# Optimization experiments

Hardware: AMD Instinct MI355X
Metric: run time of the kernel (lower is better)

Reference implementation:

```python
import jax, jax.numpy as jnp
import numpy as np

TEMPERATURE = 0.7
TOP_K = 50
TOP_P = 0.9
B, S, H, V = 2, 1024, 512, 50257


def setup_inputs() -> dict:
    key = jax.random.key(0)
    k1, k2 = jax.random.split(key)
    x = jax.random.normal(k1, (B, S, H), dtype=jnp.float32)
    # small init scale keeps logits in a realistic range so nucleus mass is spread
    W = jax.random.normal(k2, (V, H), dtype=jnp.float32) * 0.02
    b = jnp.zeros((V,), dtype=jnp.float32)
    return {"x": x, "W": W, "b": b}


def _top_k_top_p_filtering(logits):
    # --- top-k: mask everything below the k-th largest value ---
    top_k_vals = jax.lax.top_k(logits, TOP_K)[0]          # [B,S,K]
    min_top_k = top_k_vals[..., -1:]                       # [B,S,1]
    logits = jnp.where(logits < min_top_k, -jnp.inf, logits)
    # --- top-p (nucleus): sort descending, cumsum of probs, drop tail ---
    sorted_idx = jnp.argsort(-logits, axis=-1)             # descending order
    sorted_logits = jnp.take_along_axis(logits, sorted_idx, axis=-1)
    cum_probs = jnp.cumsum(jax.nn.softmax(sorted_logits, axis=-1), axis=-1)
    sorted_logits = jnp.where(cum_probs > TOP_P, -jnp.inf, sorted_logits)
    # NOTE: the original torch code does gather(sorted_logits, index=sorted_indices)
    # (forward-gather, not inverse scatter). We replicate that exact math.
    logits = jnp.take_along_axis(sorted_logits, sorted_idx, axis=-1)
    return logits


def reference(x, W, b):
    # ExampleModel: single linear projection to vocab logits [B,S,V]
    logits = jnp.einsum('bsh,vh->bsv', x, W) + b
    logits = logits / TEMPERATURE
    filtered = _top_k_top_p_filtering(logits)
    return jax.nn.softmax(filtered, axis=-1)
```

## Files before the change

kernel.cpp:

```cpp
#include <hip/hip_runtime.h>
#include <math.h>

#define TEMP 0.7f
#define TOPK 50
#define TOPP 0.9f
#define M_TOT 2048
#define K_DIM 512
#define V_DIM 50257
#define NPAD 50304
#define KP 1536
#define BM 128
#define BN 128
#define BKE 64
#define NSTEP (KP / BKE)
#define NBN (NPAD / BN)
#define NBM (M_TOT / BM)

typedef short s16x8 __attribute__((ext_vector_type(8)));
typedef float f32x4 __attribute__((ext_vector_type(4)));

#define MFMA_16x16x32_BF16(acc, va, vb) \
  asm("v_mfma_f32_16x16x32_bf16 %0, %1, %2, %0" : "+v"(acc) : "v"(va), "v"(vb))

__device__ __forceinline__ unsigned short bf16_rn(float x) {
  unsigned u = __float_as_uint(x);
  unsigned r = u + 0x7FFFu + ((u >> 16) & 1u);
  return (unsigned short)(r >> 16);
}
__device__ __forceinline__ float bf16_to_f(unsigned short h) {
  return __uint_as_float(((unsigned)h) << 16);
}
__device__ __forceinline__ unsigned f2key(float f) {
  unsigned u = __float_as_uint(f);
  return (u & 0x80000000u) ? ~u : (u | 0x80000000u);
}

__global__ __launch_bounds__(256) void convx_kernel(const float* __restrict__ X,
                                                    unsigned short* __restrict__ Xp) {
  int idx = blockIdx.x * 256 + threadIdx.x;
  const int total = M_TOT * (K_DIM / 4);
  if (idx >= total) return;
  int row = idx >> 7;
  int q = idx & 127;
  const float4 v = reinterpret_cast<const float4*>(X)[idx];
  float vv[4] = {v.x, v.y, v.z, v.w};
  unsigned short hi[4], lo[4];
#pragma unroll
  for (int j = 0; j < 4; ++j) {
    hi[j] = bf16_rn(vv[j]);
    lo[j] = bf16_rn(vv[j] - bf16_to_f(hi[j]));
  }
  ushort4 h4 = make_ushort4(hi[0], hi[1], hi[2], hi[3]);
  ushort4 l4 = make_ushort4(lo[0], lo[1], lo[2], lo[3]);
  size_t base = (size_t)row * KP + q * 4;
  *reinterpret_cast<ushort4*>(Xp + base) = h4;
  *reinterpret_cast<ushort4*>(Xp + base + K_DIM) = h4;
  *reinterpret_cast<ushort4*>(Xp + base + 2 * K_DIM) = l4;
}

__global__ __launch_bounds__(256) void convw_kernel(const float* __restrict__ W,
                                                    unsigned short* __restrict__ Wp) {
  int idx = blockIdx.x * 256 + threadIdx.x;
  const int total = NPAD * (K_DIM / 4);
  if (idx >= total) return;
  int row = idx >> 7;
  int q = idx & 127;
  float4 v = make_float4(0.f, 0.f, 0.f, 0.f);
  if (row < V_DIM) v = reinterpret_cast<const float4*>(W)[(size_t)row * 128 + q];
  float vv[4] = {v.x, v.y, v.z, v.w};
  unsigned short hi[4], lo[4];
#pragma unroll
  for (int j = 0; j < 4; ++j) {
    hi[j] = bf16_rn(vv[j]);
    lo[j] = bf16_rn(vv[j] - bf16_to_f(hi[j]));
  }
  ushort4 h4 = make_ushort4(hi[0], hi[1], hi[2], hi[3]);
  ushort4 l4 = make_ushort4(lo[0], lo[1], lo[2], lo[3]);
  size_t base = (size_t)row * KP + q * 4;
  *reinterpret_cast<ushort4*>(Wp + base) = h4;
  *reinterpret_cast<ushort4*>(Wp + base + K_DIM) = l4;
  *reinterpret_cast<ushort4*>(Wp + base + 2 * K_DIM) = h4;
}

__global__ __launch_bounds__(256) void mfma_gemm_kernel(
    const unsigned short* __restrict__ Ap, const unsigned short* __restrict__ Bp,
    const float* __restrict__ Bv, float* __restrict__ C,
    unsigned* __restrict__ Tmax) {
  __shared__ __align__(16) unsigned char lds[32768];
  __shared__ unsigned umax[BM];
  const int tid = threadIdx.x;
  const int w = tid >> 6, lane = tid & 63;
  const int bm = blockIdx.x * BM;
  const int bni = blockIdx.y;
  const int bn = bni * BN;
  const int wr = w >> 1, wc = w & 1;

  f32x4 acc[4][4] = {};

  for (int step = 0; step < NSTEP; ++step) {
    const int k0 = step * BKE;
#pragma unroll
    for (int q = 0; q < 4; ++q) {
      int pp = ((w * 4 + q) << 10) + (lane << 4);
      int row = pp >> 7;
      int cb = (pp & 127) ^ ((row & 7) << 4);
      const unsigned short* ga = Ap + (size_t)(bm + row) * KP + k0 + (cb >> 1);
      __builtin_amdgcn_global_load_lds(
          (const __attribute__((address_space(1))) unsigned int*)ga,
          (__attribute__((address_space(3))) unsigned int*)(lds + pp), 16, 0, 0);
      const unsigned short* gb = Bp + (size_t)(bn + row) * KP + k0 + (cb >> 1);
      __builtin_amdgcn_global_load_lds(
          (const __attribute__((address_space(1))) unsigned int*)gb,
          (__attribute__((address_space(3))) unsigned int*)(lds + 16384 + pp), 16, 0, 0);
    }
    __syncthreads();
#pragma unroll
    for (int kk = 0; kk < 2; ++kk) {
      const int kbyte = kk * 64 + ((lane >> 4) << 4);
      s16x8 a[4], b[4];
#pragma unroll
      for (int i = 0; i < 4; ++i) {
        int row = (wr << 6) + (i << 4) + (lane & 15);
        int byte = (row << 7) + (kbyte ^ ((row & 7) << 4));
        a[i] = *reinterpret_cast<const s16x8*>(lds + byte);
      }
#pragma unroll
      for (int j = 0; j < 4; ++j) {
        int row = (wc << 6) + (j << 4) + (lane & 15);
        int byte = (row << 7) + (kbyte ^ ((row & 7) << 4));
        b[j] = *reinterpret_cast<const s16x8*>(lds + 16384 + byte);
      }
#pragma unroll
      for (int i = 0; i < 4; ++i)
#pragma unroll
        for (int j = 0; j < 4; ++j) MFMA_16x16x32_BF16(acc[i][j], a[i], b[j]);
    }
    __syncthreads();
  }

  if (tid < BM) umax[tid] = 0;
  __syncthreads();

  float mx[4][4];
#pragma unroll
  for (int i = 0; i < 4; ++i)
#pragma unroll
    for (int r = 0; r < 4; ++r) mx[i][r] = -INFINITY;

#pragma unroll
  for (int i = 0; i < 4; ++i) {
#pragma unroll
    for (int j = 0; j < 4; ++j) {
      int n = bn + (wc << 6) + (j << 4) + (lane & 15);
      if (n < V_DIM) {
        float bv = Bv[n];
#pragma unroll
        for (int r = 0; r < 4; ++r) {
          int m = bm + (wr << 6) + (i << 4) + ((lane >> 4) << 2) + r;
          float val = (acc[i][j][r] + bv) / TEMP;
          C[(size_t)m * V_DIM + n] = val;
          mx[i][r] = fmaxf(mx[i][r], val);
        }
      }
    }
  }
#pragma unroll
  for (int i = 0; i < 4; ++i) {
#pragma unroll
    for (int r = 0; r < 4; ++r) {
      float v = mx[i][r];
      v = fmaxf(v, __shfl_xor(v, 1));
      v = fmaxf(v, __shfl_xor(v, 2));
      v = fmaxf(v, __shfl_xor(v, 4));
      v = fmaxf(v, __shfl_xor(v, 8));
      if ((lane & 15) == 0)
        atomicMax(&umax[(wr << 6) + (i << 4) + ((lane >> 4) << 2) + r], f2key(v));
    }
  }
  __syncthreads();
  if (tid < BM) Tmax[(size_t)(bm + tid) * NBN + bni] = umax[tid];
}

#define CAP 1024
#define SCAP 256

__global__ __launch_bounds__(256) void select_kernel(float* __restrict__ C,
                                                     const unsigned* __restrict__ Tmax) {
  const int row = blockIdx.x;
  float* rowp = C + (size_t)row * V_DIM;
  const int tid = threadIdx.x;

  __shared__ unsigned tk[NBN];
  __shared__ short ctile[NBN];
  __shared__ unsigned s_t50;
  __shared__ float cval[CAP];
  __shared__ int cidx[CAP];
  __shared__ float sval[SCAP];
  __shared__ int sidx[SCAP];
  __shared__ float pvals[SCAP];
  __shared__ int s_cnt, s_ntile, s_nsurv, s_kc;
  __shared__ float s_invZ;

  for (int i = tid; i < NBN; i += 256) tk[i] = Tmax[(size_t)row * NBN + i];
  if (tid == 0) { s_cnt = 0; s_ntile = 0; s_nsurv = 0; }
  __syncthreads();
  for (int i = tid; i < NBN; i += 256) {
    unsigned ki = tk[i];
    int r = 0;
    for (int j = 0; j < NBN; ++j) {
      unsigned kj = tk[j];
      r += (kj > ki) || (kj == ki && j < i);
    }
    if (r == TOPK - 1) s_t50 = ki;
  }
  __syncthreads();
  const unsigned t50 = s_t50;

  for (int i = tid; i < NBN; i += 256) {
    if (tk[i] >= t50) {
      int p = atomicAdd(&s_ntile, 1);
      ctile[p] = (short)i;
    }
  }
  __syncthreads();
  const int ntile = s_ntile;

  for (int e = tid; e < ntile * BN; e += 256) {
    int ti = ctile[e >> 7];
    int n = ti * BN + (e & 127);
    if (n < V_DIM) {
      float l = rowp[n];
      if (f2key(l) >= t50) {
        int p = atomicAdd(&s_cnt, 1);
        if (p < CAP) { cval[p] = l; cidx[p] = n; }
      }
    }
  }
  __syncthreads();
  const int n = min(s_cnt, CAP);

  {
    const float4 z4 = make_float4(0.f, 0.f, 0.f, 0.f);
    const int NQ = V_DIM >> 2;
    for (int q = tid; q < NQ; q += 256) reinterpret_cast<float4*>(rowp)[q] = z4;
    if (tid == 0) rowp[V_DIM - 1] = 0.f;
  }

  for (int i = tid; i < n; i += 256) {
    float vi = cval[i];
    int xi = cidx[i];
    int r = 0;
    for (int j = 0; j < n; ++j) {
      float vj = cval[j];
      if (vj > vi || (vj == vi && cidx[j] < xi)) ++r;
    }
    if (r < SCAP) { sval[r] = vi; sidx[r] = xi; }
  }
  __syncthreads();

  const float t = sval[TOPK - 1];
  for (int i = tid; i < n; i += 256)
    if (cval[i] >= t) atomicAdd(&s_nsurv, 1);
  __syncthreads();
  const int nsurv = min(s_nsurv, SCAP);

  const float m = sval[0];
  for (int i = tid; i < nsurv; i += 256) pvals[i] = expf(sval[i] - m);
  __syncthreads();
  if (tid == 0) {
    float Z0 = 0.f;
    for (int i = 0; i < nsurv; ++i) Z0 += pvals[i];
    float cum = 0.f;
    int kc = 0;
    float Z2 = 0.f;
    for (int i = 0; i < nsurv; ++i) {
      cum += pvals[i] / Z0;
      if (cum > TOPP) break;
      kc = i + 1;
      Z2 += pvals[i];
    }
    s_kc = kc;
    s_invZ = (kc > 0) ? (1.f / Z2) : 0.f;
  }
  __syncthreads();
  const int kc = s_kc;
  const float invZ = s_invZ;

  for (int q = tid; q < kc; q += 256) {
    int r = -1, less = 0;
    for (int s = 0; s < nsurv; ++s) {
      if (sidx[s] == q) r = s;
      if (sidx[s] < q) ++less;
    }
    int rank = (r >= 0) ? r : (nsurv + q - less);
    rowp[rank] = pvals[q] * invZ;
  }
}

extern "C" void kernel_launch(void* const* d_in, const int* in_sizes, int n_in,
                              void* d_out, int out_size, void* d_ws, size_t ws_size,
                              hipStream_t stream) {
  const float* X = (const float*)d_in[0];
  const float* W = (const float*)d_in[1];
  const float* Bv = (const float*)d_in[2];
  float* C = (float*)d_out;

  unsigned short* Xp = (unsigned short*)d_ws;
  unsigned short* Wp = Xp + (size_t)M_TOT * KP;
  unsigned* Tmax = (unsigned*)(Wp + (size_t)NPAD * KP);

  convx_kernel<<<(M_TOT * (K_DIM / 4) + 255) / 256, 256, 0, stream>>>(X, Xp);
  convw_kernel<<<(NPAD * (K_DIM / 4) + 255) / 256, 256, 0, stream>>>(W, Wp);
  dim3 g(NBM, NBN);
  mfma_gemm_kernel<<<g, 256, 0, stream>>>(Xp, Wp, Bv, C, Tmax);
  select_kernel<<<M_TOT, 256, 0, stream>>>(C, Tmax);
}
```

Before: 664.6 us.

## Replace GEMM with 256x256 tile, 8-wave double-buffered pipelined MFMA kernel

Swaps the 128x128 single-buffered GEMM for a 256x256 tile kernel with 512 threads. It double-buffers LDS (128KB) and interleaves global-to-LDS staging with quarter-tile MFMA groups under barriers and s_setprio. The goal is to hide load latency and raise arithmetic intensity per block. Per-row max reporting keeps 128-column granularity, so the select kernel's tile logic carries over with a new padded width. Risks are lower occupancy from the large LDS use, plus more padding waste in N.

```diff
diff --git a/kernel.cpp b/kernel.cpp
--- a/kernel.cpp
+++ b/kernel.cpp
@@ -7,14 +7,17 @@
 #define M_TOT 2048
 #define K_DIM 512
 #define V_DIM 50257
-#define NPAD 50304
 #define KP 1536
-#define BM 128
-#define BN 128
-#define BKE 64
-#define NSTEP (KP / BKE)
-#define NBN (NPAD / BN)
-#define NBM (M_TOT / BM)
+
+#define BM2 256
+#define BN2 256
+#define BK2 64
+#define NPAD2 50432
+#define NBN2 (NPAD2 / BN2)
+#define NBM2 (M_TOT / BM2)
+#define NKT (KP / BK2)
+#define NIT (NKT / 2)
+#define NBH (NPAD2 / 128)
 
 typedef short s16x8 __attribute__((ext_vector_type(8)));
 typedef float f32x4 __attribute__((ext_vector_type(4)));
@@ -61,7 +64,7 @@
 __global__ __launch_bounds__(256) void convw_kernel(const float* __restrict__ W,
                                                     unsigned short* __restrict__ Wp) {
   int idx = blockIdx.x * 256 + threadIdx.x;
-  const int total = NPAD * (K_DIM / 4);
+  const int total = NPAD2 * (K_DIM / 4);
   if (idx >= total) return;
   int row = idx >> 7;
   int q = idx & 127;
@@ -82,73 +85,145 @@
   *reinterpret_cast<ushort4*>(Wp + base + 2 * K_DIM) = h4;
 }
 
-__global__ __launch_bounds__(256) void mfma_gemm_kernel(
+
+#define QUAD(A, B, MH, NH)                                                   \
+  do {                                                                       \
+    __builtin_amdgcn_s_setprio(1);                                           \
+    _Pragma("unroll") for (int fi = 0; fi < 4; ++fi)                         \
+        _Pragma("unroll") for (int fj = 0; fj < 2; ++fj)                     \
+        _Pragma("unroll") for (int kk = 0; kk < 2; ++kk)                     \
+            MFMA_16x16x32_BF16(acc[(MH)*4 + fi][(NH)*2 + fj], A[fi][kk],     \
+                               B[fj][kk]);                                   \
+    __builtin_amdgcn_s_setprio(0);                                           \
+  } while (0)
+
+#define MIDBAR()                                        \
+  do {                                                  \
+    __builtin_amdgcn_s_barrier();                       \
+    asm volatile("s_waitcnt lgkmcnt(0)" ::: "memory");  \
+    __builtin_amdgcn_sched_barrier(0);                  \
+  } while (0)
+
+__global__ __launch_bounds__(512, 2) void gemm256_kernel(
     const unsigned short* __restrict__ Ap, const unsigned short* __restrict__ Bp,
     const float* __restrict__ Bv, float* __restrict__ C,
     unsigned* __restrict__ Tmax) {
-  __shared__ __align__(16) unsigned char lds[32768];
-  __shared__ unsigned umax[BM];
+  __shared__ __align__(16) unsigned char lds[131072];
   const int tid = threadIdx.x;
   const int w = tid >> 6, lane = tid & 63;
-  const int bm = blockIdx.x * BM;
-  const int bni = blockIdx.y;
-  const int bn = bni * BN;
-  const int wr = w >> 1, wc = w & 1;
-
-  f32x4 acc[4][4] = {};
-
-  for (int step = 0; step < NSTEP; ++step) {
-    const int k0 = step * BKE;
-#pragma unroll
-    for (int q = 0; q < 4; ++q) {
-      int pp = ((w * 4 + q) << 10) + (lane << 4);
+  const int wr = w >> 2, wc = w & 3;
+  const int bm = blockIdx.x * BM2, bn = blockIdx.y * BN2;
+
+  f32x4 acc[8][4] = {};
+  s16x8 a[4][2], b0[2][2], b1[2][2];
+
+  auto STAGE = [&](int kt, int part) {
+    if (kt >= NKT) return;
+    const int mat = part >> 1, half = part & 1;
+    unsigned char* base = lds + ((kt & 1) << 16) + (mat << 15);
+    const unsigned short* src = mat ? Bp : Ap;
+    const int rb = mat ? bn : bm;
+#pragma unroll
+    for (int l = 0; l < 2; ++l) {
+      int pp = (half << 14) + ((l * 512 + tid) << 4);
       int row = pp >> 7;
       int cb = (pp & 127) ^ ((row & 7) << 4);
-      const unsigned short* ga = Ap + (size_t)(bm + row) * KP + k0 + (cb >> 1);
+      const unsigned short* g = src + (size_t)(rb + row) * KP + kt * BK2 + (cb >> 1);
       __builtin_amdgcn_global_load_lds(
-          (const __attribute__((address_space(1))) unsigned int*)ga,
-          (__attribute__((address_space(3))) unsigned int*)(lds + pp), 16, 0, 0);
-      const unsigned short* gb = Bp + (size_t)(bn + row) * KP + k0 + (cb >> 1);
-      __builtin_amdgcn_global_load_lds(
-          (const __attribute__((address_space(1))) unsigned int*)gb,
-          (__attribute__((address_space(3))) unsigned int*)(lds + 16384 + pp), 16, 0, 0);
-    }
-    __syncthreads();
-#pragma unroll
-    for (int kk = 0; kk < 2; ++kk) {
-      const int kbyte = kk * 64 + ((lane >> 4) << 4);
-      s16x8 a[4], b[4];
-#pragma unroll
-      for (int i = 0; i < 4; ++i) {
-        int row = (wr << 6) + (i << 4) + (lane & 15);
-        int byte = (row << 7) + (kbyte ^ ((row & 7) << 4));
-        a[i] = *reinterpret_cast<const s16x8*>(lds + byte);
-      }
-#pragma unroll
-      for (int j = 0; j < 4; ++j) {
-        int row = (wc << 6) + (j << 4) + (lane & 15);
-        int byte = (row << 7) + (kbyte ^ ((row & 7) << 4));
-        b[j] = *reinterpret_cast<const s16x8*>(lds + 16384 + byte);
-      }
-#pragma unroll
-      for (int i = 0; i < 4; ++i)
-#pragma unroll
-        for (int j = 0; j < 4; ++j) MFMA_16x16x32_BF16(acc[i][j], a[i], b[j]);
-    }
-    __syncthreads();
-  }
-
-  if (tid < BM) umax[tid] = 0;
-  __syncthreads();
-
-  float mx[4][4];
-#pragma unroll
-  for (int i = 0; i < 4; ++i)
-#pragma unroll
-    for (int r = 0; r < 4; ++r) mx[i][r] = -INFINITY;
-
-#pragma unroll
-  for (int i = 0; i < 4; ++i) {
+          (const __attribute__((address_space(1))) unsigned int*)g,
+          (__attribute__((address_space(3))) unsigned int*)(base + pp), 16, 0, 0);
+    }
+  };
+  auto LDA = [&](int slot, int mh) {
+    const unsigned char* base = lds + (slot << 16);
+#pragma unroll
+    for (int fi = 0; fi < 4; ++fi)
+#pragma unroll
+      for (int kk = 0; kk < 2; ++kk) {
+        int row = (wr << 7) + (mh << 6) + (fi << 4) + (lane & 15);
+        int kbyte = (kk << 6) + ((lane >> 4) << 4);
+        a[fi][kk] = *reinterpret_cast<const s16x8*>(
+            base + (row << 7) + (kbyte ^ ((row & 7) << 4)));
+      }
+  };
+  auto LDB = [&](s16x8 (&b)[2][2], int slot, int nh) {
+    const unsigned char* base = lds + (slot << 16) + 32768;
+#pragma unroll
+    for (int fj = 0; fj < 2; ++fj)
+#pragma unroll
+      for (int kk = 0; kk < 2; ++kk) {
+        int col = (wc << 6) + (nh << 5) + (fj << 4) + (lane & 15);
+        int kbyte = (kk << 6) + ((lane >> 4) << 4);
+        b[fj][kk] = *reinterpret_cast<const s16x8*>(
+            base + (col << 7) + (kbyte ^ ((col & 7) << 4)));
+      }
+  };
+
+  STAGE(0, 0); STAGE(0, 1); STAGE(0, 2); STAGE(0, 3); STAGE(1, 0);
+  asm volatile("s_waitcnt vmcnt(2)" ::: "memory");
+  __builtin_amdgcn_s_barrier();
+  __builtin_amdgcn_sched_barrier(0);
+
+  for (int t = 0; t < NIT; ++t) {
+    const int k0 = 2 * t;
+    const int k1 = 2 * t + 1;
+    LDA(0, 0); LDB(b0, 0, 0);
+    STAGE(k1, 1);
+    MIDBAR();
+    QUAD(a, b0, 0, 0);
+    __builtin_amdgcn_s_barrier();
+    LDB(b1, 0, 1);
+    STAGE(k1, 2);
+    MIDBAR();
+    QUAD(a, b1, 0, 1);
+    __builtin_amdgcn_s_barrier();
+    LDA(0, 1);
+    STAGE(k1, 3);
+    MIDBAR();
+    QUAD(a, b0, 1, 0);
+    __builtin_amdgcn_s_barrier();
+    STAGE(k0 + 2, 0);
+    MIDBAR();
+    QUAD(a, b1, 1, 1);
+    if (t < NIT - 1) asm volatile("s_waitcnt vmcnt(2)" ::: "memory");
+    else             asm volatile("s_waitcnt vmcnt(0)" ::: "memory");
+    __builtin_amdgcn_s_barrier();
+    __builtin_amdgcn_sched_barrier(0);
+    LDA(1, 0); LDB(b0, 1, 0);
+    STAGE(k0 + 2, 1);
+    MIDBAR();
+    QUAD(a, b0, 0, 0);
+    __builtin_amdgcn_s_barrier();
+    LDB(b1, 1, 1);
+    STAGE(k0 + 2, 2);
+    MIDBAR();
+    QUAD(a, b1, 0, 1);
+    __builtin_amdgcn_s_barrier();
+    LDA(1, 1);
+    STAGE(k0 + 2, 3);
+    MIDBAR();
+    QUAD(a, b0, 1, 0);
+    __builtin_amdgcn_s_barrier();
+    STAGE(k1 + 2, 0);
+    MIDBAR();
+    QUAD(a, b1, 1, 1);
+    if (t < NIT - 1) asm volatile("s_waitcnt vmcnt(2)" ::: "memory");
+    else             asm volatile("s_waitcnt vmcnt(0)" ::: "memory");
+    __builtin_amdgcn_s_barrier();
+    __builtin_amdgcn_sched_barrier(0);
+  }
+
+  __syncthreads();
+  unsigned* umax = (unsigned*)lds;
+  umax[tid] = 0;
+  __syncthreads();
+
+  const int h = wc >> 1;
+#pragma unroll
+  for (int i = 0; i < 8; ++i) {
+    float mx[4];
+#pragma unroll
+    for (int r = 0; r < 4; ++r) mx[r] = -INFINITY;
 #pragma unroll
     for (int j = 0; j < 4; ++j) {
       int n = bn + (wc << 6) + (j << 4) + (lane & 15);
@@ -156,29 +231,31 @@
         float bv = Bv[n];
 #pragma unroll
         for (int r = 0; r < 4; ++r) {
-          int m = bm + (wr << 6) + (i << 4) + ((lane >> 4) << 2) + r;
+          int m = bm + (wr << 7) + (i << 4) + ((lane >> 4) << 2) + r;
           float val = (acc[i][j][r] + bv) / TEMP;
           C[(size_t)m * V_DIM + n] = val;
-          mx[i][r] = fmaxf(mx[i][r], val);
+          mx[r] = fmaxf(mx[r], val);
         }
       }
     }
-  }
-#pragma unroll
-  for (int i = 0; i < 4; ++i) {
 #pragma unroll
     for (int r = 0; r < 4; ++r) {
-      float v = mx[i][r];
+      float v = mx[r];
       v = fmaxf(v, __shfl_xor(v, 1));
       v = fmaxf(v, __shfl_xor(v, 2));
       v = fmaxf(v, __shfl_xor(v, 4));
       v = fmaxf(v, __shfl_xor(v, 8));
-      if ((lane & 15) == 0)
-        atomicMax(&umax[(wr << 6) + (i << 4) + ((lane >> 4) << 2) + r], f2key(v));
-    }
-  }
-  __syncthreads();
-  if (tid < BM) Tmax[(size_t)(bm + tid) * NBN + bni] = umax[tid];
+      if ((lane & 15) == 0) {
+        int lrow = (wr << 7) + (i << 4) + ((lane >> 4) << 2) + r;
+        atomicMax(&umax[lrow * 2 + h], f2key(v));
+      }
+    }
+  }
+  __syncthreads();
+  {
+    int lrow = tid >> 1, hh = tid & 1;
+    Tmax[(size_t)(bm + lrow) * NBH + blockIdx.y * 2 + hh] = umax[tid];
+  }
 }
 
 #define CAP 1024
@@ -190,8 +267,8 @@
   float* rowp = C + (size_t)row * V_DIM;
   const int tid = threadIdx.x;
 
-  __shared__ unsigned tk[NBN];
-  __shared__ short ctile[NBN];
+  __shared__ unsigned tk[NBH];
+  __shared__ short ctile[NBH];
   __shared__ unsigned s_t50;
   __shared__ float cval[CAP];
   __shared__ int cidx[CAP];
@@ -201,13 +278,13 @@
   __shared__ int s_cnt, s_ntile, s_nsurv, s_kc;
   __shared__ float s_invZ;
 
-  for (int i = tid; i < NBN; i += 256) tk[i] = Tmax[(size_t)row * NBN + i];
+  for (int i = tid; i < NBH; i += 256) tk[i] = Tmax[(size_t)row * NBH + i];
   if (tid == 0) { s_cnt = 0; s_ntile = 0; s_nsurv = 0; }
   __syncthreads();
-  for (int i = tid; i < NBN; i += 256) {
+  for (int i = tid; i < NBH; i += 256) {
     unsigned ki = tk[i];
     int r = 0;
-    for (int j = 0; j < NBN; ++j) {
+    for (int j = 0; j < NBH; ++j) {
       unsigned kj = tk[j];
       r += (kj > ki) || (kj == ki && j < i);
     }
@@ -216,7 +293,7 @@
   __syncthreads();
   const unsigned t50 = s_t50;
 
-  for (int i = tid; i < NBN; i += 256) {
+  for (int i = tid; i < NBH; i += 256) {
     if (tk[i] >= t50) {
       int p = atomicAdd(&s_ntile, 1);
       ctile[p] = (short)i;
@@ -225,9 +302,9 @@
   __syncthreads();
   const int ntile = s_ntile;
 
-  for (int e = tid; e < ntile * BN; e += 256) {
+  for (int e = tid; e < ntile * 128; e += 256) {
     int ti = ctile[e >> 7];
-    int n = ti * BN + (e & 127);
+    int n = ti * 128 + (e & 127);
     if (n < V_DIM) {
       float l = rowp[n];
       if (f2key(l) >= t50) {
@@ -307,11 +384,11 @@
 
   unsigned short* Xp = (unsigned short*)d_ws;
   unsigned short* Wp = Xp + (size_t)M_TOT * KP;
-  unsigned* Tmax = (unsigned*)(Wp + (size_t)NPAD * KP);
+  unsigned* Tmax = (unsigned*)(Wp + (size_t)NPAD2 * KP);
 
   convx_kernel<<<(M_TOT * (K_DIM / 4) + 255) / 256, 256, 0, stream>>>(X, Xp);
-  convw_kernel<<<(NPAD * (K_DIM / 4) + 255) / 256, 256, 0, stream>>>(W, Wp);
-  dim3 g(NBM, NBN);
-  mfma_gemm_kernel<<<g, 256, 0, stream>>>(Xp, Wp, Bv, C, Tmax);
+  convw_kernel<<<(NPAD2 * (K_DIM / 4) + 255) / 256, 256, 0, stream>>>(W, Wp);
+  dim3 g(NBM2, NBN2);
+  gemm256_kernel<<<g, 512, 0, stream>>>(Xp, Wp, Bv, C, Tmax);
   select_kernel<<<M_TOT, 256, 0, stream>>>(C, Tmax);
 }
```

New measurement: 679.8 us. 2.3% more time.
